# Kernel tuning notes

Hardware: AMD Instinct MI355X
Metric: run time of the kernel (lower is better)

The kernel has to match this reference:

```python
import jax, jax.numpy as jnp
import numpy as np

N = 50000      # num nodes
HID = 64       # hidden_dim
N2V = 64       # node2vec dim
E = 800000     # num edges
EP = 100000    # prediction edges
L = 2          # num_layers
EPS = 1e-5     # BatchNorm eps


def setup_inputs() -> dict:
    key = jax.random.key(0)
    ks = jax.random.split(key, 8)
    edge_index = jax.random.randint(ks[0], (2, E), 0, N)
    pred_edge = jax.random.randint(ks[1], (EP, 2), 0, N)
    id_emb = jax.random.normal(ks[2], (N, HID), jnp.float32) * 0.1      # learnable ID embedding
    n2v_emb = jax.random.normal(ks[3], (N, N2V), jnp.float32) * 0.1     # frozen node2vec embedding
    proj_w = jax.random.normal(ks[4], (HID + N2V, HID), jnp.float32) / np.sqrt(HID + N2V)
    proj_b = jnp.zeros((HID,), jnp.float32)
    conv_w = jax.random.normal(ks[5], (L, HID, HID), jnp.float32) / np.sqrt(HID)
    conv_b = jnp.zeros((L, HID), jnp.float32)
    bn_gamma = jnp.ones((L, HID), jnp.float32)
    bn_beta = jnp.zeros((L, HID), jnp.float32)
    return {"edge_index": edge_index, "pred_edge": pred_edge, "id_emb": id_emb,
            "n2v_emb": n2v_emb, "proj_w": proj_w, "proj_b": proj_b,
            "conv_w": conv_w, "conv_b": conv_b, "bn_gamma": bn_gamma, "bn_beta": bn_beta}


def reference(edge_index, pred_edge, id_emb, n2v_emb, proj_w, proj_b, conv_w, conv_b, bn_gamma, bn_beta):
    # input projection of concatenated embeddings: [N, HID+N2V] @ [HID+N2V, HID]
    x = jnp.concatenate([id_emb, n2v_emb], axis=1) @ proj_w + proj_b

    # GCN normalization with self-loops: norm_e = d^-1/2[src] * d^-1/2[dst]
    loops = jnp.arange(N, dtype=edge_index.dtype)
    row = jnp.concatenate([edge_index[0], loops])   # source nodes
    col = jnp.concatenate([edge_index[1], loops])   # destination nodes
    deg = jax.ops.segment_sum(jnp.ones(row.shape, x.dtype), col, num_segments=N)
    dis = jnp.where(deg > 0, jax.lax.rsqrt(deg), 0.0)
    norm = dis[row] * dis[col]                      # [E+N]

    for l in range(L):
        h = x @ conv_w[l]                                                    # [N, HID]
        agg = jax.ops.segment_sum(norm[:, None] * h[row], col, num_segments=N) + conv_b[l]
        # BatchNorm1d (training-mode batch stats over nodes)
        mu = agg.mean(axis=0)
        var = agg.var(axis=0)
        xn = (agg - mu) * jax.lax.rsqrt(var + EPS) * bn_gamma[l] + bn_beta[l]
        x = x + jax.nn.relu(xn)                                              # residual (shapes match)

    # dot-product link decoder
    z = x
    return (z[pred_edge[:, 0]] * z[pred_edge[:, 1]]).sum(axis=1)
```

## Files before the change

### kernel.cpp

```cpp
#include <hip/hip_runtime.h>

#define NN 50000
#define HID 64
#define NE 800000
#define NP 100000
#define BN_EPS 1e-5f
#define NB1 196
#define MAXDEG 96

static inline size_t alignup(size_t x) { return (x + 255) & ~(size_t)255; }

__device__ __forceinline__ void f4fma(float a, const float4& w, float4& c) {
    c.x += a * w.x; c.y += a * w.y; c.z += a * w.z; c.w += a * w.w;
}
__device__ __forceinline__ void f4add(const float4& a, float4& c) {
    c.x += a.x; c.y += a.y; c.z += a.z; c.w += a.w;
}
__device__ __forceinline__ unsigned bfpack(float a, float b) {
    unsigned ua = __float_as_uint(a), ub = __float_as_uint(b);
    ua = (ua + 0x7fffu + ((ua >> 16) & 1u)) >> 16;
    ub = (ub + 0x7fffu + ((ub >> 16) & 1u)) >> 16;
    return ua | (ub << 16);
}
__device__ __forceinline__ float4 bf2f4(uint2 u) {
    float4 r;
    r.x = __uint_as_float(u.x << 16);
    r.y = __uint_as_float(u.x & 0xffff0000u);
    r.z = __uint_as_float(u.y << 16);
    r.w = __uint_as_float(u.y & 0xffff0000u);
    return r;
}


__global__ __launch_bounds__(256) void k_zero(int* __restrict__ cnt, float* __restrict__ sums) {
    int i = blockIdx.x * blockDim.x + threadIdx.x;
    if (i < NN) cnt[i] = 0;
    if (i < 256) sums[i] = 0.f;
}


__global__ __launch_bounds__(256) void k_count(const int* __restrict__ col,
                                               int* __restrict__ cnt, int* __restrict__ rank) {
    int e = blockIdx.x * blockDim.x + threadIdx.x;
    if (e < NE) rank[e] = atomicAdd(&cnt[col[e]], 1);
}


__global__ __launch_bounds__(256) void k_fill(const int* __restrict__ row, const int* __restrict__ col,
                                              const int* __restrict__ rank,
                                              unsigned short* __restrict__ csr) {
    int e = blockIdx.x * blockDim.x + threadIdx.x;
    if (e >= NE) return;
    csr[col[e] * MAXDEG + rank[e]] = (unsigned short)row[e];
}


__global__ __launch_bounds__(256) void k_proj(const float* __restrict__ id_emb,
                                              const float* __restrict__ n2v,
                                              const float* __restrict__ W,
                                              const float* __restrict__ b,
                                              const int* __restrict__ cnt,
                                              float* __restrict__ x,
                                              unsigned short* __restrict__ xh) {
    __shared__ unsigned short Wlh[128 * 64];
    __shared__ unsigned short Al[32 * 132];
    int tid = threadIdx.x;
    int node0 = blockIdx.x * 32;
    const float2* W2f = (const float2*)W;
#pragma unroll
    for (int it = 0; it < 16; ++it) {
        int i = it * 256 + tid;
        float2 w = W2f[i];
        *(unsigned*)&Wlh[2 * i] = bfpack(w.x, w.y);
    }
    const float2* id2 = (const float2*)id_emb;
    const float2* nv2 = (const float2*)n2v;
#pragma unroll
    for (int it = 0; it < 8; ++it) {
        int i = it * 256 + tid;
        int r = i >> 6, kp = i & 63;
        int n = node0 + r;
        float2 v = make_float2(0.f, 0.f);
        if (n < NN) v = (kp < 32) ? id2[n * 32 + kp] : nv2[n * 32 + (kp - 32)];
        *(unsigned*)&Al[r * 132 + 2 * kp] = bfpack(v.x, v.y);
    }
    __syncthreads();
    int sub = tid >> 4, q = tid & 15;
    const uint2* W2 = (const uint2*)Wlh;
    float4* x4 = (float4*)x;
    uint2* xh2 = (uint2*)xh;
    float4 bb = ((const float4*)b)[q];
    float4 c0 = bb, c1 = bb;
#pragma unroll 4
    for (int k4 = 0; k4 < 32; ++k4) {
        float4 w0 = bf2f4(W2[(k4 * 4 + 0) * 16 + q]);
        float4 w1 = bf2f4(W2[(k4 * 4 + 1) * 16 + q]);
        float4 w2 = bf2f4(W2[(k4 * 4 + 2) * 16 + q]);
        float4 w3 = bf2f4(W2[(k4 * 4 + 3) * 16 + q]);
        float4 a0 = bf2f4(*(const uint2*)&Al[(sub * 2 + 0) * 132 + k4 * 4]);
        float4 a1 = bf2f4(*(const uint2*)&Al[(sub * 2 + 1) * 132 + k4 * 4]);
        f4fma(a0.x, w0, c0); f4fma(a0.y, w1, c0); f4fma(a0.z, w2, c0); f4fma(a0.w, w3, c0);
        f4fma(a1.x, w0, c1); f4fma(a1.y, w1, c1); f4fma(a1.z, w2, c1); f4fma(a1.w, w3, c1);
    }
    int n0 = node0 + sub * 2;
    if (n0 + 0 < NN) { float d = rsqrtf((float)(cnt[n0+0] + 1)); x4[(n0+0)*16+q] = c0;
        xh2[(n0+0)*16+q] = make_uint2(bfpack(c0.x*d,c0.y*d), bfpack(c0.z*d,c0.w*d)); }
    if (n0 + 1 < NN) { float d = rsqrtf((float)(cnt[n0+1] + 1)); x4[(n0+1)*16+q] = c1;
        xh2[(n0+1)*16+q] = make_uint2(bfpack(c1.x*d,c1.y*d), bfpack(c1.z*d,c1.w*d)); }
}


__global__ __launch_bounds__(256) void k_gather(const int* __restrict__ cnt,
                                                const unsigned short* __restrict__ csr,
                                                const unsigned short* __restrict__ xh,
                                                unsigned short* __restrict__ th) {
    int gw = (blockIdx.x * blockDim.x + threadIdx.x) >> 6;
    int lane = threadIdx.x & 63;
    int sub = lane >> 4, q = lane & 15;
    int node = gw * 4 + sub;
    if (node >= NN) return;
    const uint2* xh2 = (const uint2*)xh;
    float4 acc = make_float4(0.f, 0.f, 0.f, 0.f);
    const unsigned short* cs = csr + node * MAXDEG;
    int c = cnt[node];
    int jj = 0;
    for (; jj + 7 < c; jj += 8) {
        uint4 s8 = *(const uint4*)(cs + jj);
        int s0 = s8.x & 0xffff, s1 = s8.x >> 16;
        int s2 = s8.y & 0xffff, s3 = s8.y >> 16;
        int s4 = s8.z & 0xffff, s5 = s8.z >> 16;
        int s6 = s8.w & 0xffff, s7 = s8.w >> 16;
        uint2 u0 = xh2[s0 * 16 + q];
        uint2 u1 = xh2[s1 * 16 + q];
        uint2 u2 = xh2[s2 * 16 + q];
        uint2 u3 = xh2[s3 * 16 + q];
        uint2 u4 = xh2[s4 * 16 + q];
        uint2 u5 = xh2[s5 * 16 + q];
        uint2 u6 = xh2[s6 * 16 + q];
        uint2 u7 = xh2[s7 * 16 + q];
        f4add(bf2f4(u0), acc); f4add(bf2f4(u1), acc);
        f4add(bf2f4(u2), acc); f4add(bf2f4(u3), acc);
        f4add(bf2f4(u4), acc); f4add(bf2f4(u5), acc);
        f4add(bf2f4(u6), acc); f4add(bf2f4(u7), acc);
    }
    for (; jj < c; ++jj) {
        uint2 u0 = xh2[cs[jj] * 16 + q];
        f4add(bf2f4(u0), acc);
    }
    f4add(bf2f4(xh2[node * 16 + q]), acc);
    float di = rsqrtf((float)(c + 1));
    acc.x *= di; acc.y *= di; acc.z *= di; acc.w *= di;
    ((uint2*)th)[node * 16 + q] = make_uint2(bfpack(acc.x, acc.y), bfpack(acc.z, acc.w));
}


__global__ __launch_bounds__(256) void k_gemm_stats(const unsigned short* __restrict__ th,
                                                    const float* __restrict__ W,
                                                    unsigned short* __restrict__ agg,
                                                    float* __restrict__ sums) {
    __shared__ float Wl[64 * 64];
    __shared__ float ls0[16][64];
    __shared__ float ls1[16][64];
    int tid = threadIdx.x;
    for (int i = tid; i < 64 * 64; i += 256) Wl[i] = W[i];
    __syncthreads();
    int sub = tid >> 4, q = tid & 15;
    const uint2* t2 = (const uint2*)th;
    const float4* W4 = (const float4*)Wl;
    uint2* agg2 = (uint2*)agg;
    float4 s1 = make_float4(0.f, 0.f, 0.f, 0.f), s2 = s1;
#pragma unroll
    for (int gg = 0; gg < 2; ++gg) {
        int g = blockIdx.x * 2 + gg;
        int n0 = g * 64 + sub * 4;
        int r0 = min(n0 + 0, NN - 1), r1 = min(n0 + 1, NN - 1);
        int r2 = min(n0 + 2, NN - 1), r3 = min(n0 + 3, NN - 1);
        float4 c0 = make_float4(0.f,0.f,0.f,0.f), c1 = c0, c2 = c0, c3 = c0;
#pragma unroll 4
        for (int k4 = 0; k4 < 16; ++k4) {
            float4 a0 = bf2f4(t2[r0 * 16 + k4]);
            float4 a1 = bf2f4(t2[r1 * 16 + k4]);
            float4 a2 = bf2f4(t2[r2 * 16 + k4]);
            float4 a3 = bf2f4(t2[r3 * 16 + k4]);
            float4 w0 = W4[(k4 * 4 + 0) * 16 + q];
            float4 w1 = W4[(k4 * 4 + 1) * 16 + q];
            float4 w2 = W4[(k4 * 4 + 2) * 16 + q];
            float4 w3 = W4[(k4 * 4 + 3) * 16 + q];
            f4fma(a0.x, w0, c0); f4fma(a0.y, w1, c0); f4fma(a0.z, w2, c0); f4fma(a0.w, w3, c0);
            f4fma(a1.x, w0, c1); f4fma(a1.y, w1, c1); f4fma(a1.z, w2, c1); f4fma(a1.w, w3, c1);
            f4fma(a2.x, w0, c2); f4fma(a2.y, w1, c2); f4fma(a2.z, w2, c2); f4fma(a2.w, w3, c2);
            f4fma(a3.x, w0, c3); f4fma(a3.y, w1, c3); f4fma(a3.z, w2, c3); f4fma(a3.w, w3, c3);
        }
        if (n0 + 0 < NN) { agg2[(n0 + 0) * 16 + q] = make_uint2(bfpack(c0.x, c0.y), bfpack(c0.z, c0.w));
            s1.x += c0.x; s1.y += c0.y; s1.z += c0.z; s1.w += c0.w;
            s2.x += c0.x*c0.x; s2.y += c0.y*c0.y; s2.z += c0.z*c0.z; s2.w += c0.w*c0.w; }
        if (n0 + 1 < NN) { agg2[(n0 + 1) * 16 + q] = make_uint2(bfpack(c1.x, c1.y), bfpack(c1.z, c1.w));
            s1.x += c1.x; s1.y += c1.y; s1.z += c1.z; s1.w += c1.w;
            s2.x += c1.x*c1.x; s2.y += c1.y*c1.y; s2.z += c1.z*c1.z; s2.w += c1.w*c1.w; }
        if (n0 + 2 < NN) { agg2[(n0 + 2) * 16 + q] = make_uint2(bfpack(c2.x, c2.y), bfpack(c2.z, c2.w));
            s1.x += c2.x; s1.y += c2.y; s1.z += c2.z; s1.w += c2.w;
            s2.x += c2.x*c2.x; s2.y += c2.y*c2.y; s2.z += c2.z*c2.z; s2.w += c2.w*c2.w; }
        if (n0 + 3 < NN) { agg2[(n0 + 3) * 16 + q] = make_uint2(bfpack(c3.x, c3.y), bfpack(c3.z, c3.w));
            s1.x += c3.x; s1.y += c3.y; s1.z += c3.z; s1.w += c3.w;
            s2.x += c3.x*c3.x; s2.y += c3.y*c3.y; s2.z += c3.z*c3.z; s2.w += c3.w*c3.w; }
    }
    ls0[sub][q * 4 + 0] = s1.x; ls0[sub][q * 4 + 1] = s1.y;
    ls0[sub][q * 4 + 2] = s1.z; ls0[sub][q * 4 + 3] = s1.w;
    ls1[sub][q * 4 + 0] = s2.x; ls1[sub][q * 4 + 1] = s2.y;
    ls1[sub][q * 4 + 2] = s2.z; ls1[sub][q * 4 + 3] = s2.w;
    __syncthreads();
    if (tid < 64) {
        float a = 0.f;
#pragma unroll
        for (int r = 0; r < 16; ++r) a += ls0[r][tid];
        atomicAdd(&sums[tid], a);
    } else if (tid < 128) {
        int c = tid - 64;
        float a = 0.f;
#pragma unroll
        for (int r = 0; r < 16; ++r) a += ls1[r][c];
        atomicAdd(&sums[64 + c], a);
    }
}


__global__ __launch_bounds__(256) void k_bnupdate(const unsigned short* __restrict__ agg,
                                                  const float* __restrict__ sums,
                                                  const float* __restrict__ gamma,
                                                  const float* __restrict__ beta,
                                                  const int* __restrict__ cnt,
                                                  int prescale,
                                                  float* __restrict__ x,
                                                  unsigned short* __restrict__ xh) {
    int i = blockIdx.x * blockDim.x + threadIdx.x;
    if (i >= NN * 16) return;
    int f4 = i & 15;
    const float invn = 1.0f / (float)NN;
    float4 sm = ((const float4*)sums)[f4];
    float4 sq = ((const float4*)(sums + 64))[f4];
    float4 g = ((const float4*)gamma)[f4];
    float4 be = ((const float4*)beta)[f4];
    float4 a = bf2f4(((const uint2*)agg)[i]);
    float4 xv = ((const float4*)x)[i];
    float mu, var, rstd, xn;
    mu = sm.x * invn; var = sq.x * invn - mu * mu; rstd = rsqrtf(var + BN_EPS);
    xn = (a.x - mu) * rstd * g.x + be.x; xv.x += fmaxf(xn, 0.f);
    mu = sm.y * invn; var = sq.y * invn - mu * mu; rstd = rsqrtf(var + BN_EPS);
    xn = (a.y - mu) * rstd * g.y + be.y; xv.y += fmaxf(xn, 0.f);
    mu = sm.z * invn; var = sq.z * invn - mu * mu; rstd = rsqrtf(var + BN_EPS);
    xn = (a.z - mu) * rstd * g.z + be.z; xv.z += fmaxf(xn, 0.f);
    mu = sm.w * invn; var = sq.w * invn - mu * mu; rstd = rsqrtf(var + BN_EPS);
    xn = (a.w - mu) * rstd * g.w + be.w; xv.w += fmaxf(xn, 0.f);
    if (prescale) {
        ((float4*)x)[i] = xv;
        float d = rsqrtf((float)(cnt[i >> 4] + 1));
        ((uint2*)xh)[i] = make_uint2(bfpack(xv.x * d, xv.y * d), bfpack(xv.z * d, xv.w * d));
    } else {
        ((uint2*)xh)[i] = make_uint2(bfpack(xv.x, xv.y), bfpack(xv.z, xv.w));
    }
}


__global__ __launch_bounds__(256) void k_decode(const int* __restrict__ pred,
                                                const unsigned short* __restrict__ zh,
                                                float* __restrict__ out) {
    int gw = (blockIdx.x * blockDim.x + threadIdx.x) >> 6;
    int lane = threadIdx.x & 63;
    int sub = lane >> 4, q = lane & 15;
    int p = gw * 4 + sub;
    if (p >= NP) return;
    const uint2* z2 = (const uint2*)zh;
    int a = pred[2 * p], b = pred[2 * p + 1];
    float4 va = bf2f4(z2[a * 16 + q]);
    float4 vb = bf2f4(z2[b * 16 + q]);
    float v = va.x * vb.x + va.y * vb.y + va.z * vb.z + va.w * vb.w;
    v += __shfl_xor(v, 1);
    v += __shfl_xor(v, 2);
    v += __shfl_xor(v, 4);
    v += __shfl_xor(v, 8);
    if (q == 0) out[p] = v;
}

extern "C" void kernel_launch(void* const* d_in, const int* in_sizes, int n_in,
                              void* d_out, int out_size, void* d_ws, size_t ws_size,
                              hipStream_t stream) {
    const int* edge_index = (const int*)d_in[0];
    const int* pred       = (const int*)d_in[1];
    const float* id_emb   = (const float*)d_in[2];
    const float* n2v      = (const float*)d_in[3];
    const float* proj_w   = (const float*)d_in[4];
    const float* proj_b   = (const float*)d_in[5];
    const float* conv_w   = (const float*)d_in[6];
    const float* gamma    = (const float*)d_in[8];
    const float* beta     = (const float*)d_in[9];
    float* out = (float*)d_out;

    char* ws = (char*)d_ws;
    size_t off = 0;
    int* cnt     = (int*)(ws + off);   off += alignup(NN * 4);
    int* rank    = (int*)(ws + off);   off += alignup((size_t)NE * 4);
    unsigned short* csr = (unsigned short*)(ws + off); off += alignup((size_t)NN * MAXDEG * 2);
    float* x     = (float*)(ws + off); off += alignup((size_t)NN * 64 * 4);
    unsigned short* agg = (unsigned short*)(ws + off); off += alignup((size_t)NN * 64 * 2);
    unsigned short* xh = (unsigned short*)(ws + off); off += alignup((size_t)NN * 64 * 2);
    unsigned short* th = (unsigned short*)(ws + off); off += alignup((size_t)NN * 64 * 2);
    float* sums  = (float*)(ws + off);

    const int* row = edge_index;
    const int* col = edge_index + NE;

    k_zero<<<NB1, 256, 0, stream>>>(cnt, sums);
    k_count<<<(NE + 255) / 256, 256, 0, stream>>>(col, cnt, rank);
    k_fill<<<(NE + 255) / 256, 256, 0, stream>>>(row, col, rank, csr);

    k_proj<<<(NN + 31) / 32, 256, 0, stream>>>(id_emb, n2v, proj_w, proj_b, cnt, x, xh);

    for (int l = 0; l < 2; ++l) {
        k_gather<<<((NN + 3) / 4 * 64 + 255) / 256, 256, 0, stream>>>(cnt, csr, xh, th);
        k_gemm_stats<<<391, 256, 0, stream>>>(th, conv_w + l * 64 * 64, agg, sums + l * 128);
        k_bnupdate<<<(NN * 16 + 255) / 256, 256, 0, stream>>>(agg, sums + l * 128, gamma + l * 64,
                                                              beta + l * 64, cnt, (l == 0) ? 1 : 0, x, xh);
    }

    k_decode<<<(NP / 4 * 64 + 255) / 256, 256, 0, stream>>>(pred, xh, out);
}
```

Before: 186.6 us.

## Use bf16 MFMA for per-layer GEMM and shrink rank buffer to bytes

Rewrites k_gemm_stats to run the 64x64 per-layer matmul on MFMA 16x16x32 bf16 instructions, one wave per 16 nodes. The weights are converted to bf16 and stored transposed in padded shared memory, and the per-column BN statistics are reduced with wave shuffles instead of a 16-row shared-memory pass. The kernel now launches 782 blocks of 64 nodes instead of 391 blocks of 128. Separately, the per-edge rank array shrinks from int to unsigned char to cut memory traffic in count/fill, which relies on degree staying below 256. The weights are now rounded to bf16, which loses precision, and agg is written with scattered 2-byte stores rather than packed 8-byte ones.

```diff
diff --git a/kernel.cpp b/kernel.cpp
--- a/kernel.cpp
+++ b/kernel.cpp
@@ -10,6 +10,9 @@
 
 static inline size_t alignup(size_t x) { return (x + 255) & ~(size_t)255; }
 
+typedef __attribute__((ext_vector_type(8))) short bf16x8;
+typedef __attribute__((ext_vector_type(4))) float f32x4;
+
 __device__ __forceinline__ void f4fma(float a, const float4& w, float4& c) {
     c.x += a * w.x; c.y += a * w.y; c.z += a * w.z; c.w += a * w.w;
 }
@@ -21,6 +24,10 @@
     ua = (ua + 0x7fffu + ((ua >> 16) & 1u)) >> 16;
     ub = (ub + 0x7fffu + ((ub >> 16) & 1u)) >> 16;
     return ua | (ub << 16);
+}
+__device__ __forceinline__ unsigned short bf1(float a) {
+    unsigned ua = __float_as_uint(a);
+    return (unsigned short)((ua + 0x7fffu + ((ua >> 16) & 1u)) >> 16);
 }
 __device__ __forceinline__ float4 bf2f4(uint2 u) {
     float4 r;
@@ -40,18 +47,18 @@
 
 
 __global__ __launch_bounds__(256) void k_count(const int* __restrict__ col,
-                                               int* __restrict__ cnt, int* __restrict__ rank) {
+                                               int* __restrict__ cnt, unsigned char* __restrict__ rank) {
     int e = blockIdx.x * blockDim.x + threadIdx.x;
-    if (e < NE) rank[e] = atomicAdd(&cnt[col[e]], 1);
+    if (e < NE) rank[e] = (unsigned char)atomicAdd(&cnt[col[e]], 1);
 }
 
 
 __global__ __launch_bounds__(256) void k_fill(const int* __restrict__ row, const int* __restrict__ col,
-                                              const int* __restrict__ rank,
+                                              const unsigned char* __restrict__ rank,
                                               unsigned short* __restrict__ csr) {
     int e = blockIdx.x * blockDim.x + threadIdx.x;
     if (e >= NE) return;
-    csr[col[e] * MAXDEG + rank[e]] = (unsigned short)row[e];
+    csr[col[e] * MAXDEG + (int)rank[e]] = (unsigned short)row[e];
 }
 
 
@@ -158,67 +165,61 @@
                                                     const float* __restrict__ W,
                                                     unsigned short* __restrict__ agg,
                                                     float* __restrict__ sums) {
-    __shared__ float Wl[64 * 64];
-    __shared__ float ls0[16][64];
-    __shared__ float ls1[16][64];
+    __shared__ unsigned short Wt[64 * 72];
+    __shared__ float ls0[4][64];
+    __shared__ float ls1[4][64];
     int tid = threadIdx.x;
-    for (int i = tid; i < 64 * 64; i += 256) Wl[i] = W[i];
+#pragma unroll
+    for (int it = 0; it < 16; ++it) {
+        int i = it * 256 + tid;
+        int k = i >> 6, n = i & 63;
+        Wt[n * 72 + k] = bf1(W[i]);
+    }
     __syncthreads();
-    int sub = tid >> 4, q = tid & 15;
-    const uint2* t2 = (const uint2*)th;
-    const float4* W4 = (const float4*)Wl;
-    uint2* agg2 = (uint2*)agg;
-    float4 s1 = make_float4(0.f, 0.f, 0.f, 0.f), s2 = s1;
-#pragma unroll
-    for (int gg = 0; gg < 2; ++gg) {
-        int g = blockIdx.x * 2 + gg;
-        int n0 = g * 64 + sub * 4;
-        int r0 = min(n0 + 0, NN - 1), r1 = min(n0 + 1, NN - 1);
-        int r2 = min(n0 + 2, NN - 1), r3 = min(n0 + 3, NN - 1);
-        float4 c0 = make_float4(0.f,0.f,0.f,0.f), c1 = c0, c2 = c0, c3 = c0;
-#pragma unroll 4
-        for (int k4 = 0; k4 < 16; ++k4) {
-            float4 a0 = bf2f4(t2[r0 * 16 + k4]);
-            float4 a1 = bf2f4(t2[r1 * 16 + k4]);
-            float4 a2 = bf2f4(t2[r2 * 16 + k4]);
-            float4 a3 = bf2f4(t2[r3 * 16 + k4]);
-            float4 w0 = W4[(k4 * 4 + 0) * 16 + q];
-            float4 w1 = W4[(k4 * 4 + 1) * 16 + q];
-            float4 w2 = W4[(k4 * 4 + 2) * 16 + q];
-            float4 w3 = W4[(k4 * 4 + 3) * 16 + q];
-            f4fma(a0.x, w0, c0); f4fma(a0.y, w1, c0); f4fma(a0.z, w2, c0); f4fma(a0.w, w3, c0);
-            f4fma(a1.x, w0, c1); f4fma(a1.y, w1, c1); f4fma(a1.z, w2, c1); f4fma(a1.w, w3, c1);
-            f4fma(a2.x, w0, c2); f4fma(a2.y, w1, c2); f4fma(a2.z, w2, c2); f4fma(a2.w, w3, c2);
-            f4fma(a3.x, w0, c3); f4fma(a3.y, w1, c3); f4fma(a3.z, w2, c3); f4fma(a3.w, w3, c3);
+    int wave = tid >> 6, lane = tid & 63;
+    int n0w = blockIdx.x * 64 + wave * 16;
+    int arow = lane & 15;
+    int kgrp = lane >> 4;
+    int anode = min(n0w + arow, NN - 1);
+    const bf16x8* thv = (const bf16x8*)th;
+    bf16x8 a0 = thv[anode * 8 + kgrp];
+    bf16x8 a1 = thv[anode * 8 + 4 + kgrp];
+    const bf16x8* wtv = (const bf16x8*)Wt;
+    f32x4 acc[4];
+#pragma unroll
+    for (int ct = 0; ct < 4; ++ct) {
+        int bro = (ct * 16 + arow) * 9;
+        bf16x8 b0 = wtv[bro + kgrp];
+        bf16x8 b1 = wtv[bro + 4 + kgrp];
+        f32x4 c = {0.f, 0.f, 0.f, 0.f};
+        c = __builtin_amdgcn_mfma_f32_16x16x32_bf16(a0, b0, c, 0, 0, 0);
+        c = __builtin_amdgcn_mfma_f32_16x16x32_bf16(a1, b1, c, 0, 0, 0);
+        acc[ct] = c;
+    }
+#pragma unroll
+    for (int ct = 0; ct < 4; ++ct) {
+        float p1 = 0.f, p2 = 0.f;
+#pragma unroll
+        for (int j = 0; j < 4; ++j) {
+            int node = n0w + kgrp * 4 + j;
+            float v = acc[ct][j];
+            if (node < NN) {
+                agg[node * 64 + ct * 16 + arow] = bf1(v);
+                p1 += v;
+                p2 += v * v;
+            }
         }
-        if (n0 + 0 < NN) { agg2[(n0 + 0) * 16 + q] = make_uint2(bfpack(c0.x, c0.y), bfpack(c0.z, c0.w));
-            s1.x += c0.x; s1.y += c0.y; s1.z += c0.z; s1.w += c0.w;
-            s2.x += c0.x*c0.x; s2.y += c0.y*c0.y; s2.z += c0.z*c0.z; s2.w += c0.w*c0.w; }
-        if (n0 + 1 < NN) { agg2[(n0 + 1) * 16 + q] = make_uint2(bfpack(c1.x, c1.y), bfpack(c1.z, c1.w));
-            s1.x += c1.x; s1.y += c1.y; s1.z += c1.z; s1.w += c1.w;
-            s2.x += c1.x*c1.x; s2.y += c1.y*c1.y; s2.z += c1.z*c1.z; s2.w += c1.w*c1.w; }
-        if (n0 + 2 < NN) { agg2[(n0 + 2) * 16 + q] = make_uint2(bfpack(c2.x, c2.y), bfpack(c2.z, c2.w));
-            s1.x += c2.x; s1.y += c2.y; s1.z += c2.z; s1.w += c2.w;
-            s2.x += c2.x*c2.x; s2.y += c2.y*c2.y; s2.z += c2.z*c2.z; s2.w += c2.w*c2.w; }
-        if (n0 + 3 < NN) { agg2[(n0 + 3) * 16 + q] = make_uint2(bfpack(c3.x, c3.y), bfpack(c3.z, c3.w));
-            s1.x += c3.x; s1.y += c3.y; s1.z += c3.z; s1.w += c3.w;
-            s2.x += c3.x*c3.x; s2.y += c3.y*c3.y; s2.z += c3.z*c3.z; s2.w += c3.w*c3.w; }
-    }
-    ls0[sub][q * 4 + 0] = s1.x; ls0[sub][q * 4 + 1] = s1.y;
-    ls0[sub][q * 4 + 2] = s1.z; ls0[sub][q * 4 + 3] = s1.w;
-    ls1[sub][q * 4 + 0] = s2.x; ls1[sub][q * 4 + 1] = s2.y;
-    ls1[sub][q * 4 + 2] = s2.z; ls1[sub][q * 4 + 3] = s2.w;
+        p1 += __shfl_xor(p1, 16); p2 += __shfl_xor(p2, 16);
+        p1 += __shfl_xor(p1, 32); p2 += __shfl_xor(p2, 32);
+        if (kgrp == 0) { ls0[wave][ct * 16 + arow] = p1; ls1[wave][ct * 16 + arow] = p2; }
+    }
     __syncthreads();
     if (tid < 64) {
-        float a = 0.f;
-#pragma unroll
-        for (int r = 0; r < 16; ++r) a += ls0[r][tid];
+        float a = ls0[0][tid] + ls0[1][tid] + ls0[2][tid] + ls0[3][tid];
         atomicAdd(&sums[tid], a);
     } else if (tid < 128) {
         int c = tid - 64;
-        float a = 0.f;
-#pragma unroll
-        for (int r = 0; r < 16; ++r) a += ls1[r][c];
+        float a = ls1[0][c] + ls1[1][c] + ls1[2][c] + ls1[3][c];
         atomicAdd(&sums[64 + c], a);
     }
 }
@@ -298,12 +299,12 @@
     char* ws = (char*)d_ws;
     size_t off = 0;
     int* cnt     = (int*)(ws + off);   off += alignup(NN * 4);
-    int* rank    = (int*)(ws + off);   off += alignup((size_t)NE * 4);
+    unsigned char* rank = (unsigned char*)(ws + off); off += alignup((size_t)NE);
     unsigned short* csr = (unsigned short*)(ws + off); off += alignup((size_t)NN * MAXDEG * 2);
     float* x     = (float*)(ws + off); off += alignup((size_t)NN * 64 * 4);
     unsigned short* agg = (unsigned short*)(ws + off); off += alignup((size_t)NN * 64 * 2);
     unsigned short* xh = (unsigned short*)(ws + off); off += alignup((size_t)NN * 64 * 2);
-    unsigned short* th = (unsigned short*)(ws + off); off += alignup((size_t)NN * 64 * 2);
+    unsigned short* th = (unsigned short*)(ws + off); off += alignup((size_t)(NN * 64 + 64) * 2);
     float* sums  = (float*)(ws + off);
 
     const int* row = edge_index;
@@ -317,7 +318,7 @@
 
     for (int l = 0; l < 2; ++l) {
         k_gather<<<((NN + 3) / 4 * 64 + 255) / 256, 256, 0, stream>>>(cnt, csr, xh, th);
-        k_gemm_stats<<<391, 256, 0, stream>>>(th, conv_w + l * 64 * 64, agg, sums + l * 128);
+        k_gemm_stats<<<(NN + 63) / 64, 256, 0, stream>>>(th, conv_w + l * 64 * 64, agg, sums + l * 128);
         k_bnupdate<<<(NN * 16 + 255) / 256, 256, 0, stream>>>(agg, sums + l * 128, gamma + l * 64,
                                                               beta + l * 64, cnt, (l == 0) ? 1 : 0, x, xh);
     }
```

After: 192.2 us. +3.0%, slower.
